# Kernel optimization log

Hardware: AMD Instinct MI355X
Metric: run time of the kernel (lower is better)

The kernel has to match this reference:

```python
import jax, jax.numpy as jnp
import numpy as np

B, NF, S, L, H, MID, KS, NC, DENSE = 16, 8, 16, 256, 128, 32, 8, 10, 512
COEFF = 0.1
BN_EPS = 1e-5


def _normalize(x):
    return x / jnp.maximum(jnp.linalg.norm(x, axis=-1, keepdims=True), 1e-12)


def _sparsemax(z):
    # sparsemax over last axis (Martins & Astudillo 2016)
    zs = jnp.flip(jnp.sort(z, axis=-1), axis=-1)
    k = jnp.arange(1, z.shape[-1] + 1, dtype=z.dtype)
    cum = jnp.cumsum(zs, axis=-1)
    support = (1.0 + k * zs) > cum
    ksup = jnp.sum(support, axis=-1, keepdims=True)
    tau = (jnp.take_along_axis(cum, ksup - 1, axis=-1) - 1.0) / ksup.astype(z.dtype)
    return jnp.maximum(z - tau, 0.0)


def _bn_ncl(x, g, b, m, v):  # eval-mode BatchNorm1d on [N, C, L]
    return g[None, :, None] * (x - m[None, :, None]) * jax.lax.rsqrt(v[None, :, None] + BN_EPS) + b[None, :, None]


def _bn_nc(x, g, b, m, v):  # eval-mode BatchNorm1d on [N, C]
    return g * (x - m) * jax.lax.rsqrt(v + BN_EPS) + b


def _conv(x, w, pad):
    return jax.lax.conv_general_dilated(x, w, (1,), [(pad, pad)], dimension_numbers=('NCH', 'OIH', 'NCH'))


def _maxpool2(x):  # MaxPool1d(kernel=2, stride=2, padding=1): -inf padded
    return jax.lax.reduce_window(x, -jnp.inf, jax.lax.max, (1, 1, 2), (1, 1, 2), ((0, 0), (0, 0), (1, 1)))


def _cnn(x, cw1, bn1, cw2, bn2, cw3, bn3):
    x = _maxpool2(jax.nn.relu(_bn_ncl(_conv(x, cw1, KS // 2), *bn1)))
    x = _maxpool2(jax.nn.relu(_bn_ncl(_conv(x, cw2, 4), *bn2)))
    x = _maxpool2(jax.nn.relu(_bn_ncl(_conv(x, cw3, 4), *bn3)))
    return jnp.mean(x, axis=-1)  # AdaptiveAvgPool1d(1) -> [N, H]


def _alpha_beta(x, cw1, bn1, cw2, bn2, cw3, bn3, Wq, bq, Wk, bk, Wv, bv):
    b = x.shape[0]
    xf = jnp.transpose(x, (1, 0, 2, 3)).reshape(NF, b * S, 1, L)
    rep = jax.vmap(_cnn)(xf, cw1, bn1, cw2, bn2, cw3, bn3)  # [F, B*S, H]
    rep = rep.reshape(NF, b, S, H)
    Q = jax.nn.elu(rep @ Wq + bq)
    K = jax.nn.leaky_relu(rep @ Wk + bk)
    V = jax.nn.leaky_relu(rep @ Wv + bv)
    # mean_t(Q @ K^T) == Q @ mean_t(K); then scale by sqrt(d_k)
    scores = jnp.einsum('fbsh,fbh->fbs', Q, jnp.mean(K, axis=2)) / jnp.sqrt(jnp.float32(H))
    intra_aw = _sparsemax(scores)                             # [F, B, S]
    Z = _normalize(jnp.einsum('fbs,fbsh->fbh', intra_aw, V))  # [F, B, H]
    Kn = _normalize(rep)
    inter_scores = jnp.einsum('ibh,fbsh->ifbs', Z, Kn)        # cosine scores (Z already unit-norm)
    inter_aw = _sparsemax(inter_scores)                       # [I, F, B, S]
    U = jnp.einsum('ifbs,fbsh->ibh', inter_aw, rep) / NF      # mean over feature axis f
    Hc = _normalize(jnp.concatenate([Z, U], axis=-1))         # [F, B, 2H]
    feat = jnp.transpose(Hc, (1, 0, 2)).reshape(b, NF * 2 * H)
    return feat, intra_aw, inter_aw


def _forward(src_x, src_y, tgt_x, cw1, bn1_g, bn1_b, bn1_m, bn1_v, cw2, bn2_g, bn2_b, bn2_m, bn2_v, cw3, bn3_g, bn3_b, bn3_m, bn3_v, Wq, bq, Wk, bk, Wv, bv, bnc1_g, bnc1_b, bnc1_m, bnc1_v, W1, b1, bnc2_g, bnc2_b, bnc2_m, bnc2_v, W2, b2):
    bn1 = (bn1_g, bn1_b, bn1_m, bn1_v)
    bn2 = (bn2_g, bn2_b, bn2_m, bn2_v)
    bn3 = (bn3_g, bn3_b, bn3_m, bn3_v)
    sf, sa, sb = _alpha_beta(src_x, cw1, bn1, cw2, bn2, cw3, bn3, Wq, bq, Wk, bk, Wv, bv)
    _, ta, tb = _alpha_beta(tgt_x, cw1, bn1, cw2, bn2, cw3, bn3, Wq, bq, Wk, bk, Wv, bv)
    h = _bn_nc(sf, bnc1_g, bnc1_b, bnc1_m, bnc1_v) @ W1 + b1
    h = jax.nn.leaky_relu(_bn_nc(h, bnc2_g, bnc2_b, bnc2_m, bnc2_v))
    y_pred = jax.nn.softmax(h @ W2 + b2, axis=-1)
    # MMD domain losses (detached in original via torch.tensor(list))
    da = jnp.mean(sa - ta, axis=-2)                           # [F, S]
    loss_a = COEFF * jnp.mean(jnp.linalg.norm(da, axis=-1))
    db = jnp.mean(sb - tb, axis=-2)                           # [I, F, S]
    loss_b = COEFF * jnp.mean(jnp.sqrt(jnp.sum(db * db, axis=(1, 2))))
    dom = jax.lax.stop_gradient(loss_a + loss_b)
    # CrossEntropyLoss applied to already-softmaxed preds, as in source
    logp = jax.nn.log_softmax(y_pred, axis=-1)
    ce = -jnp.mean(logp[jnp.arange(y_pred.shape[0]), src_y])
    return y_pred, ce + dom


def setup_inputs() -> dict:
    ks = jax.random.split(jax.random.key(0), 40)
    rn = lambda i, sh, s=1.0: s * jax.random.normal(ks[i], sh, dtype=jnp.float32)
    ru = lambda i, sh, lo, hi: jax.random.uniform(ks[i], sh, jnp.float32, lo, hi)
    return {
        'src_x': rn(0, (B, NF, S, L)),
        'src_y': jax.random.randint(ks[1], (B,), 0, NC),
        'tgt_x': rn(2, (B, NF, S, L)),
        'cw1': rn(3, (NF, MID, 1, KS), 0.1),
        'bn1_g': ru(4, (NF, MID), 0.75, 1.25), 'bn1_b': rn(5, (NF, MID), 0.1),
        'bn1_m': rn(6, (NF, MID), 0.1), 'bn1_v': ru(7, (NF, MID), 0.5, 1.5),
        'cw2': rn(8, (NF, 2 * MID, MID, 8), 0.05),
        'bn2_g': ru(9, (NF, 2 * MID), 0.75, 1.25), 'bn2_b': rn(10, (NF, 2 * MID), 0.1),
        'bn2_m': rn(11, (NF, 2 * MID), 0.1), 'bn2_v': ru(12, (NF, 2 * MID), 0.5, 1.5),
        'cw3': rn(13, (NF, H, 2 * MID, 8), 0.05),
        'bn3_g': ru(14, (NF, H), 0.75, 1.25), 'bn3_b': rn(15, (NF, H), 0.1),
        'bn3_m': rn(16, (NF, H), 0.1), 'bn3_v': ru(17, (NF, H), 0.5, 1.5),
        'Wq': rn(18, (H, H), 0.05), 'bq': rn(19, (H,), 0.02),
        'Wk': rn(20, (H, H), 0.05), 'bk': rn(21, (H,), 0.02),
        'Wv': rn(22, (H, H), 0.05), 'bv': rn(23, (H,), 0.02),
        'bnc1_g': ru(24, (NF * 2 * H,), 0.75, 1.25), 'bnc1_b': rn(25, (NF * 2 * H,), 0.1),
        'bnc1_m': rn(26, (NF * 2 * H,), 0.1), 'bnc1_v': ru(27, (NF * 2 * H,), 0.5, 1.5),
        'W1': rn(28, (NF * 2 * H, DENSE), 0.03), 'b1': rn(29, (DENSE,), 0.02),
        'bnc2_g': ru(30, (DENSE,), 0.75, 1.25), 'bnc2_b': rn(31, (DENSE,), 0.1),
        'bnc2_m': rn(32, (DENSE,), 0.1), 'bnc2_v': ru(33, (DENSE,), 0.5, 1.5),
        'W2': rn(34, (DENSE, NC), 0.05), 'b2': rn(35, (NC,), 0.02),
    }


def reference(src_x, src_y, tgt_x, cw1, bn1_g, bn1_b, bn1_m, bn1_v, cw2, bn2_g, bn2_b, bn2_m, bn2_v, cw3, bn3_g, bn3_b, bn3_m, bn3_v, Wq, bq, Wk, bk, Wv, bv, bnc1_g, bnc1_b, bnc1_m, bnc1_v, W1, b1, bnc2_g, bnc2_b, bnc2_m, bnc2_v, W2, b2):
    return _forward(src_x, src_y, tgt_x, cw1, bn1_g, bn1_b, bn1_m, bn1_v, cw2, bn2_g, bn2_b, bn2_m, bn2_v, cw3, bn3_g, bn3_b, bn3_m, bn3_v, Wq, bq, Wk, bk, Wv, bv, bnc1_g, bnc1_b, bnc1_m, bnc1_v, W1, b1, bnc2_g, bnc2_b, bnc2_m, bnc2_v, W2, b2)
```

## Files before the change

kernel.cpp:

```cpp
#include <hip/hip_runtime.h>

typedef unsigned short u16;
typedef unsigned int u32;
typedef __attribute__((ext_vector_type(8))) short bfrag;
typedef __attribute__((ext_vector_type(4))) float ffrag;

__device__ __forceinline__ float lrelu(float x) { return x >= 0.f ? x : 0.01f * x; }
__device__ __forceinline__ float eluf(float x)  { return x > 0.f ? x : expm1f(x); }
__device__ __forceinline__ u16 f2bf(float f) {
    u32 x = __float_as_uint(f);
    return (u16)((x + 0x7fffu + ((x >> 16) & 1u)) >> 16);
}
__device__ __forceinline__ u16 f2bt(float f) {
    return (u16)(__float_as_uint(f) >> 16);
}
__device__ __forceinline__ float bf2f(u16 u) {
    return __uint_as_float(((u32)u) << 16);
}

__device__ void sparsemax16(const float* z, float* out) {
    float zs[16];
    for (int i = 0; i < 16; ++i) zs[i] = z[i];
    for (int i = 1; i < 16; ++i) {
        float key = zs[i]; int j = i - 1;
        while (j >= 0 && zs[j] < key) { zs[j + 1] = zs[j]; --j; }
        zs[j + 1] = key;
    }
    float cum[16];
    cum[0] = zs[0];
    for (int i = 1; i < 16; ++i) cum[i] = cum[i - 1] + zs[i];
    int ksup = 0;
    for (int k = 1; k <= 16; ++k)
        if (1.0f + (float)k * zs[k - 1] > cum[k - 1]) ksup++;
    if (ksup < 1) ksup = 1;
    float tau = (cum[ksup - 1] - 1.0f) / (float)ksup;
    for (int i = 0; i < 16; ++i) out[i] = fmaxf(z[i] - tau, 0.0f);
}

__global__ __launch_bounds__(256) void k_wprep(
    const float* __restrict__ w2, const float* __restrict__ w3,
    const float* __restrict__ Wq, const float* __restrict__ Wk,
    const float* __restrict__ Wv,
    u16* __restrict__ wpk2, u16* __restrict__ wpk3, u16* __restrict__ wqkv)
{
    int i = blockIdx.x * 256 + threadIdx.x;
    if (i < 131072) {
        int j = i & 7, L = (i >> 3) & 63, kc = (i >> 9) & 7, nt = (i >> 12) & 3, f = i >> 14;
        int co = nt * 16 + (L & 15);
        int ci = ((L >> 4) << 3) + j;
        wpk2[i] = f2bf(w2[(((size_t)f * 64 + co) * 32 + ci) * 8 + kc]);
    } else if (i < 131072 + 524288) {
        int i2 = i - 131072;
        int j = i2 & 7, L = (i2 >> 3) & 63, kc = (i2 >> 9) & 15, nt = (i2 >> 13) & 7, f = i2 >> 16;
        int co = nt * 16 + (L & 15);
        int ci = ((kc & 1) << 5) + ((L >> 4) << 3) + j;
        wpk3[i2] = f2bf(w3[(((size_t)f * 128 + co) * 64 + ci) * 8 + (kc >> 1)]);
    } else if (i < 131072 + 524288 + 49152) {
        int j2 = i - 655360;
        int proj = j2 >> 14, idx = j2 & 16383;
        int jj = idx & 7, L = (idx >> 3) & 63, kc = (idx >> 9) & 3, nt = idx >> 11;
        int n = nt * 16 + (L & 15);
        int k = kc * 32 + ((L >> 4) << 3) + jj;
        const float* W = proj == 0 ? Wq : (proj == 1 ? Wk : Wv);
        wqkv[j2] = f2bf(W[k * 128 + n]);
    }
}

#define S1T_STRIDE 40
#define S2T_STRIDE 72
#define RB2_STRIDE 68
#define RB3_STRIDE 140
#define RB_OFF 6336
#define SMEM_U16 (RB_OFF + 67 * RB3_STRIDE)

__global__ __launch_bounds__(256) void k_cnn(
    const float* __restrict__ xs, const float* __restrict__ xt,
    const float* __restrict__ w1, const float* __restrict__ g1, const float* __restrict__ b1,
    const float* __restrict__ m1, const float* __restrict__ v1,
    const float* __restrict__ g2, const float* __restrict__ b2,
    const float* __restrict__ m2, const float* __restrict__ v2,
    const float* __restrict__ g3, const float* __restrict__ b3,
    const float* __restrict__ m3, const float* __restrict__ v3,
    const u16* __restrict__ wpk2, const u16* __restrict__ wpk3,
    float* __restrict__ rep)
{
    __shared__ __align__(16) u16 smem[SMEM_U16];
    float* xin = (float*)(smem + RB_OFF);

    int tid = threadIdx.x, blk = blockIdx.x;
    int pass = blk >> 11, f = (blk >> 8) & 7, n = blk & 255;
    int bb = n >> 4, ss = n & 15;
    int lane = tid & 63, w = tid >> 6;
    const float* x = pass ? xt : xs;
    float* rep_p = rep + (size_t)pass * 262144;

    {
        u32* z = (u32*)smem;
        for (int i = tid; i < 3168; i += 256) z[i] = 0;
        for (int i = tid; i < 264; i += 256) xin[i] = 0.f;
    }
    __syncthreads();
    {
        const float* xr = x + (((size_t)bb * 8 + f) * 16 + ss) * 256;
        for (int i = tid; i < 256; i += 256) xin[i + 4] = xr[i];
    }
    __syncthreads();

    if (tid < 208) {
        int cc = tid & 7, jc = tid >> 3;
        int co0 = cc * 4, j0 = jc * 5;
        float wr[4][8];
        for (int c = 0; c < 4; ++c) {
            const float4* q = reinterpret_cast<const float4*>(w1 + ((size_t)f * 32 + co0 + c) * 8);
            float4 a = q[0], bq = q[1];
            wr[c][0] = a.x; wr[c][1] = a.y; wr[c][2] = a.z; wr[c][3] = a.w;
            wr[c][4] = bq.x; wr[c][5] = bq.y; wr[c][6] = bq.z; wr[c][7] = bq.w;
        }
        int px[10];
        for (int i = 0; i < 10; ++i) {
            int p = 2 * j0 - 1 + i;
            px[i] = p < 0 ? 0 : (p > 256 ? 256 : p);
        }
        float acc[4][10];
        for (int c = 0; c < 4; ++c) for (int i = 0; i < 10; ++i) acc[c][i] = 0.f;
        for (int k = 0; k < 8; ++k) {
            float xv[10];
            for (int i = 0; i < 10; ++i) xv[i] = xin[px[i] + k];
            for (int c = 0; c < 4; ++c)
                for (int i = 0; i < 10; ++i) acc[c][i] += wr[c][k] * xv[i];
        }
        for (int c = 0; c < 4; ++c) {
            int co = co0 + c;
            float sc = g1[f * 32 + co] * rsqrtf(v1[f * 32 + co] + 1e-5f);
            float sh = b1[f * 32 + co] - m1[f * 32 + co] * sc;
            for (int jj = 0; jj < 5; ++jj) {
                int j = j0 + jj;
                if (j < 129) {
                    float a0 = fmaxf(acc[c][2 * jj] * sc + sh, 0.f);
                    float a1 = fmaxf(acc[c][2 * jj + 1] * sc + sh, 0.f);
                    smem[(j + 4) * S1T_STRIDE + co] = f2bt(fmaxf(a0, a1));
                }
            }
        }
    }
    __syncthreads();

    {
        int nt = w;
        bfrag B2[8];
        const bfrag* gB = reinterpret_cast<const bfrag*>(wpk2);
        for (int kc = 0; kc < 8; ++kc)
            B2[kc] = gB[(((size_t)f * 4 + nt) * 8 + kc) * 64 + lane];
        int co = nt * 16 + (lane & 15);
        float sc = g2[f * 64 + co] * rsqrtf(v2[f * 64 + co] + 1e-5f);
        float sh = b2[f * 64 + co] - m2[f * 64 + co] * sc;
        int arow = lane & 15, ci0 = (lane >> 4) << 3;
        for (int mt = 0; mt < 9; ++mt) {
            ffrag C = {0.f, 0.f, 0.f, 0.f};
            int rb = mt * 16 + arow;
            for (int kc = 0; kc < 8; ++kc) {
                bfrag A = *reinterpret_cast<const bfrag*>(&smem[(rb + kc) * S1T_STRIDE + ci0]);
                C = __builtin_amdgcn_mfma_f32_16x16x32_bf16(A, B2[kc], C, 0, 0, 0);
            }
            int p0 = mt * 16 + ((lane >> 4) << 2);
            for (int r = 0; r < 4; ++r) {
                int p = p0 + r;
                if (p < 130)
                    smem[RB_OFF + p * RB2_STRIDE + co] = f2bt(fmaxf(C[r] * sc + sh, 0.f));
            }
        }
    }
    __syncthreads();

    {
        u32* z = (u32*)smem;
        for (int i = tid; i < 3168; i += 256) z[i] = 0;
    }
    __syncthreads();

    for (int e = tid; e < 66 * 64; e += 256) {
        int j = e >> 6, ci = e & 63;
        float vmax;
        if (j == 0) {
            vmax = bf2f(smem[RB_OFF + 0 * RB2_STRIDE + ci]);
        } else if (j == 65) {
            vmax = bf2f(smem[RB_OFF + 129 * RB2_STRIDE + ci]);
        } else {
            float a0 = bf2f(smem[RB_OFF + (2 * j - 1) * RB2_STRIDE + ci]);
            float a1 = bf2f(smem[RB_OFF + (2 * j) * RB2_STRIDE + ci]);
            vmax = fmaxf(a0, a1);
        }
        smem[(j + 4) * S2T_STRIDE + ci] = f2bt(vmax);
    }
    __syncthreads();

    for (int t = 0; t < 2; ++t) {
        int nt = w * 2 + t;
        bfrag B3[16];
        const bfrag* gB = reinterpret_cast<const bfrag*>(wpk3);
        for (int kc = 0; kc < 16; ++kc)
            B3[kc] = gB[(((size_t)f * 8 + nt) * 16 + kc) * 64 + lane];
        int co = nt * 16 + (lane & 15);
        float sc = g3[f * 128 + co] * rsqrtf(v3[f * 128 + co] + 1e-5f);
        float sh = b3[f * 128 + co] - m3[f * 128 + co] * sc;
        int arow = lane & 15, q8 = (lane >> 4) << 3;
        for (int mt = 0; mt < 5; ++mt) {
            ffrag C = {0.f, 0.f, 0.f, 0.f};
            int rb = mt * 16 + arow;
            for (int kc = 0; kc < 16; ++kc) {
                int row = rb + (kc >> 1);
                int ci0 = ((kc & 1) << 5) + q8;
                bfrag A = *reinterpret_cast<const bfrag*>(&smem[row * S2T_STRIDE + ci0]);
                C = __builtin_amdgcn_mfma_f32_16x16x32_bf16(A, B3[kc], C, 0, 0, 0);
            }
            int p0 = mt * 16 + ((lane >> 4) << 2);
            for (int r = 0; r < 4; ++r) {
                int p = p0 + r;
                if (p < 67)
                    smem[RB_OFF + p * RB3_STRIDE + co] = f2bt(fmaxf(C[r] * sc + sh, 0.f));
            }
        }
    }
    __syncthreads();

    if (tid < 128) {
        int co = tid;
        float sum = bf2f(smem[RB_OFF + 0 * RB3_STRIDE + co]);
        for (int j = 1; j < 34; ++j) {
            float a0 = bf2f(smem[RB_OFF + (2 * j - 1) * RB3_STRIDE + co]);
            float a1 = bf2f(smem[RB_OFF + (2 * j) * RB3_STRIDE + co]);
            sum += fmaxf(a0, a1);
        }
        rep_p[(((size_t)f * 256) + n) * 128 + co] = sum * (1.0f / 34.0f);
    }
}

__global__ __launch_bounds__(256) void k_attn1(
    const float* __restrict__ rep, const u16* __restrict__ wqkv,
    const float* __restrict__ bq, const float* __restrict__ bk,
    const float* __restrict__ bv,
    float* __restrict__ Zn, float* __restrict__ rninv, float* __restrict__ iaw)
{
    __shared__ __align__(16) u16 repbf[16 * 136];
    __shared__ float KmL[128], ZL[128], awL[16], scoresL[16], r2L[16];
    __shared__ float spart[4][4][4];
    __shared__ float redL[4];
    int tid = threadIdx.x;
    int pass = blockIdx.x >> 7, f = (blockIdx.x >> 4) & 7, b = blockIdx.x & 15;
    const float* rp = rep + (size_t)pass * 262144 + ((size_t)f * 256 + b * 16) * 128;
    float* Zn_p = Zn + (size_t)pass * 16384;
    float* rninv_p = rninv + (size_t)pass * 2048;
    float* iaw_p = iaw + (size_t)pass * 2048;

    {
        int s = tid >> 4, i = tid & 15, h0 = i * 8;
        const float4* q4 = reinterpret_cast<const float4*>(rp + s * 128 + h0);
        float4 a = q4[0], c = q4[1];
        float p2 = a.x*a.x + a.y*a.y + a.z*a.z + a.w*a.w
                 + c.x*c.x + c.y*c.y + c.z*c.z + c.w*c.w;
        bfrag pk;
        pk[0] = (short)f2bt(a.x); pk[1] = (short)f2bt(a.y);
        pk[2] = (short)f2bt(a.z); pk[3] = (short)f2bt(a.w);
        pk[4] = (short)f2bt(c.x); pk[5] = (short)f2bt(c.y);
        pk[6] = (short)f2bt(c.z); pk[7] = (short)f2bt(c.w);
        *reinterpret_cast<bfrag*>(&repbf[s * 136 + h0]) = pk;
        p2 += __shfl_xor(p2, 1); p2 += __shfl_xor(p2, 2);
        p2 += __shfl_xor(p2, 4); p2 += __shfl_xor(p2, 8);
        if (i == 0) r2L[s] = p2;
    }
    __syncthreads();

    int lane = tid & 63, w = tid >> 6, arow = lane & 15, q = lane >> 4;
    bfrag A[4];
    for (int kc = 0; kc < 4; ++kc)
        A[kc] = *reinterpret_cast<const bfrag*>(&repbf[arow * 136 + kc * 32 + q * 8]);

    float qv[2][4], vvv[2][4];
    int colv[2];
    const bfrag* BB = reinterpret_cast<const bfrag*>(wqkv);
    for (int t = 0; t < 2; ++t) {
        int nt = w * 2 + t;
        ffrag cq = {0.f,0.f,0.f,0.f}, ck = {0.f,0.f,0.f,0.f}, cv = {0.f,0.f,0.f,0.f};
        for (int kc = 0; kc < 4; ++kc) {
            int fi = (nt * 4 + kc) * 64 + lane;
            bfrag Bq = BB[fi];
            bfrag Bk = BB[2048 + fi];
            bfrag Bv = BB[4096 + fi];
            cq = __builtin_amdgcn_mfma_f32_16x16x32_bf16(A[kc], Bq, cq, 0, 0, 0);
            ck = __builtin_amdgcn_mfma_f32_16x16x32_bf16(A[kc], Bk, ck, 0, 0, 0);
            cv = __builtin_amdgcn_mfma_f32_16x16x32_bf16(A[kc], Bv, cv, 0, 0, 0);
        }
        int col = nt * 16 + arow;
        colv[t] = col;
        float bqc = bq[col], bkc = bk[col], bvc = bv[col];
        float kpt = 0.f;
        for (int r = 0; r < 4; ++r) {
            qv[t][r] = eluf(cq[r] + bqc);
            vvv[t][r] = lrelu(cv[r] + bvc);
            kpt += lrelu(ck[r] + bkc);
        }
        kpt += __shfl_xor(kpt, 16);
        kpt += __shfl_xor(kpt, 32);
        if (q == 0) KmL[col] = kpt * (1.f / 16.f);
    }
    __syncthreads();

    {
        float km0 = KmL[colv[0]], km1 = KmL[colv[1]];
        float ps[4];
        for (int r = 0; r < 4; ++r) {
            float v = qv[0][r] * km0 + qv[1][r] * km1;
            v += __shfl_xor(v, 1); v += __shfl_xor(v, 2);
            v += __shfl_xor(v, 4); v += __shfl_xor(v, 8);
            ps[r] = v;
        }
        if (arow == 0)
            for (int r = 0; r < 4; ++r) spart[w][q][r] = ps[r];
    }
    __syncthreads();
    if (tid < 16) {
        int qq = tid >> 2, rr = tid & 3;
        float sc = spart[0][qq][rr] + spart[1][qq][rr] + spart[2][qq][rr] + spart[3][qq][rr];
        scoresL[tid] = sc * 0.08838834764831845f;
        rninv_p[f * 256 + b * 16 + tid] = 1.f / fmaxf(sqrtf(r2L[tid]), 1e-12f);
    }
    __syncthreads();
    if (tid == 0) sparsemax16(scoresL, awL);
    __syncthreads();
    if (tid < 16) iaw_p[f * 256 + b * 16 + tid] = awL[tid];

    for (int t = 0; t < 2; ++t) {
        float zp = 0.f;
        for (int r = 0; r < 4; ++r) zp += awL[q * 4 + r] * vvv[t][r];
        zp += __shfl_xor(zp, 16);
        zp += __shfl_xor(zp, 32);
        if (q == 0) ZL[colv[t]] = zp;
    }
    __syncthreads();
    if (tid < 128) {
        float z = ZL[tid];
        float v = z * z;
        v += __shfl_xor(v, 1); v += __shfl_xor(v, 2); v += __shfl_xor(v, 4);
        v += __shfl_xor(v, 8); v += __shfl_xor(v, 16); v += __shfl_xor(v, 32);
        if (lane == 0) redL[w] = v;
    }
    __syncthreads();
    if (tid == 0) redL[2] = 1.f / fmaxf(sqrtf(redL[0] + redL[1]), 1e-12f);
    __syncthreads();
    if (tid < 128)
        Zn_p[((size_t)f * 16 + b) * 128 + tid] = ZL[tid] * redL[2];
}

__global__ __launch_bounds__(256) void k_attn2(
    const float* __restrict__ rep, const float* __restrict__ Zn,
    const float* __restrict__ rninv, float* __restrict__ ibw,
    const float* __restrict__ g, const float* __restrict__ bb,
    const float* __restrict__ mm, const float* __restrict__ vv,
    float* __restrict__ featbn)
{
    __shared__ float repL[16384];
    __shared__ float ZiL[128], scores[128], UL[128];
    __shared__ float awLf[8][16];
    __shared__ float redL[2];
    int tid = threadIdx.x, blk = blockIdx.x;
    int pass = blk >> 7, b = (blk >> 3) & 15, i = blk & 7;
    const float* rep_p = rep + (size_t)pass * 262144;

    for (int f = 0; f < 8; ++f) {
        const float4* src = reinterpret_cast<const float4*>(
            rep_p + ((size_t)f * 256 + b * 16) * 128);
        float4* dst = reinterpret_cast<float4*>(repL + f * 2048);
        for (int t = tid; t < 512; t += 256) dst[t] = src[t];
    }
    if (tid < 128) ZiL[tid] = Zn[(size_t)pass * 16384 + ((size_t)i * 16 + b) * 128 + tid];
    __syncthreads();

    if (tid < 128) {
        int f = tid >> 4, s = tid & 15;
        const float* rr = repL + tid * 128;
        float a = 0.f;
        for (int h = 0; h < 128; ++h) a += ZiL[h] * rr[h];
        scores[tid] = a * rninv[(size_t)pass * 2048 + f * 256 + b * 16 + s];
    }
    __syncthreads();
    if (tid < 8) {
        float aw[16];
        sparsemax16(&scores[tid * 16], aw);
        for (int s = 0; s < 16; ++s) awLf[tid][s] = aw[s];
    }
    __syncthreads();
    if (tid < 128) {
        int f = tid >> 4, s = tid & 15;
        ibw[(size_t)pass * 16384 + (((size_t)i * 8 + f) * 16 + b) * 16 + s] = awLf[f][s];
    }
    if (pass == 0) {
        if (tid < 128) {
            int h = tid;
            float u = 0.f;
            for (int f = 0; f < 8; ++f) {
                const float* rr = repL + f * 2048 + h;
                const float* aa = awLf[f];
                for (int s = 0; s < 16; ++s) u += aa[s] * rr[s * 128];
            }
            UL[h] = u * 0.125f;
        }
        __syncthreads();
        if (tid < 128) {
            int lane = tid & 63, w = tid >> 6;
            float v = ZiL[tid] * ZiL[tid] + UL[tid] * UL[tid];
            v += __shfl_xor(v, 1); v += __shfl_xor(v, 2); v += __shfl_xor(v, 4);
            v += __shfl_xor(v, 8); v += __shfl_xor(v, 16); v += __shfl_xor(v, 32);
            if (lane == 0) redL[w] = v;
        }
        __syncthreads();
        if (tid < 256) {
            float inv = 1.f / fmaxf(sqrtf(redL[0] + redL[1]), 1e-12f);
            int d = tid;
            int e = i * 256 + d;
            float val = (d < 128 ? ZiL[d] : UL[d - 128]) * inv;
            float scv = g[e] * rsqrtf(vv[e] + 1e-5f);
            featbn[b * 2048 + e] = (val - mm[e]) * scv + bb[e];
        }
    }
}

__global__ __launch_bounds__(256) void k_head1(
    const float* __restrict__ featbn,
    const float* __restrict__ W1, const float* __restrict__ b1,
    const float* __restrict__ g2, const float* __restrict__ bb2,
    const float* __restrict__ mm2, const float* __restrict__ vv2,
    float* __restrict__ h2ws)
{
    __shared__ float featL[2048];
    __shared__ float part[32][32];
    int tid = threadIdx.x, blk = blockIdx.x;
    int b = blk >> 4, cc = blk & 15;
    {
        const float4* src = reinterpret_cast<const float4*>(featbn + b * 2048);
        float4* dst = reinterpret_cast<float4*>(featL);
        for (int i = tid; i < 512; i += 256) dst[i] = src[i];
    }
    __syncthreads();
    int ks = tid >> 3, cg = tid & 7;
    int col0 = cc * 32 + cg * 4;
    float4 acc = {0.f, 0.f, 0.f, 0.f};
    const float* fl = featL + ks * 64;
    for (int c = 0; c < 64; ++c) {
        int k = ks * 64 + c;
        float4 wv = *reinterpret_cast<const float4*>(W1 + (size_t)k * 512 + col0);
        float fv = fl[c];
        acc.x += fv * wv.x; acc.y += fv * wv.y;
        acc.z += fv * wv.z; acc.w += fv * wv.w;
    }
    part[ks][cg * 4 + 0] = acc.x;
    part[ks][cg * 4 + 1] = acc.y;
    part[ks][cg * 4 + 2] = acc.z;
    part[ks][cg * 4 + 3] = acc.w;
    __syncthreads();
    if (tid < 32) {
        int colw = cc * 32 + tid;
        float s = b1[colw];
        for (int k2 = 0; k2 < 32; ++k2) s += part[k2][tid];
        float scv = g2[colw] * rsqrtf(vv2[colw] + 1e-5f);
        float val = (s - mm2[colw]) * scv + bb2[colw];
        h2ws[b * 512 + colw] = lrelu(val);
    }
}

__global__ __launch_bounds__(256) void k_tail(
    const float* __restrict__ h2ws,
    const float* __restrict__ W2, const float* __restrict__ b2,
    const float* __restrict__ sa, const float* __restrict__ ta,
    const float* __restrict__ sb, const float* __restrict__ tb,
    const int* __restrict__ sy, float* __restrict__ dout)
{
    __shared__ float h2L[8192];
    __shared__ float lgL[160], ypL[160];
    __shared__ float sA[8], sB[8];
    int tid = threadIdx.x;
    for (int i = tid; i < 8192; i += 256) h2L[i] = h2ws[i];
    if (tid < 8) { sA[tid] = 0.f; sB[tid] = 0.f; }
    __syncthreads();
    if (tid < 160) {
        int b = tid / 10, j = tid - b * 10;
        float a = b2[j];
        const float* h = h2L + b * 512;
        for (int c = 0; c < 512; ++c) a += h[c] * W2[c * 10 + j];
        lgL[tid] = a;
    }
    __syncthreads();
    if (tid < 16) {
        int b = tid;
        float mx = lgL[b * 10];
        for (int j = 1; j < 10; ++j) mx = fmaxf(mx, lgL[b * 10 + j]);
        float sum = 0.f, ex[10];
        for (int j = 0; j < 10; ++j) { ex[j] = expf(lgL[b * 10 + j] - mx); sum += ex[j]; }
        for (int j = 0; j < 10; ++j) {
            float p = ex[j] / sum;
            ypL[b * 10 + j] = p;
            dout[b * 10 + j] = p;
        }
    }
    __syncthreads();
    if (tid < 128) {
        int f = tid >> 4, s = tid & 15;
        float d = 0.f;
        for (int b = 0; b < 16; ++b) d += sa[f * 256 + b * 16 + s] - ta[f * 256 + b * 16 + s];
        d *= (1.f / 16.f);
        atomicAdd(&sA[f], d * d);
    }
    for (int e = tid; e < 1024; e += 256) {
        int i = e >> 7, f = (e >> 4) & 7, s = e & 15;
        float d = 0.f;
        int base = ((i * 8 + f) * 16) * 16 + s;
        for (int b = 0; b < 16; ++b) d += sb[base + b * 16] - tb[base + b * 16];
        d *= (1.f / 16.f);
        atomicAdd(&sB[i], d * d);
    }
    __syncthreads();
    if (tid == 0) {
        float la = 0.f, lb = 0.f;
        for (int f = 0; f < 8; ++f) la += sqrtf(sA[f]);
        for (int i = 0; i < 8; ++i) lb += sqrtf(sB[i]);
        la *= 0.1f / 8.f;
        lb *= 0.1f / 8.f;
        float ce = 0.f;
        for (int b = 0; b < 16; ++b) {
            const float* y = ypL + b * 10;
            float mx = y[0];
            for (int j = 1; j < 10; ++j) mx = fmaxf(mx, y[j]);
            float sum = 0.f;
            for (int j = 0; j < 10; ++j) sum += expf(y[j] - mx);
            float lse = mx + logf(sum);
            ce += lse - y[sy[b]];
        }
        ce *= (1.f / 16.f);
        dout[160] = ce + la + lb;
    }
}

extern "C" void kernel_launch(void* const* d_in, const int* in_sizes, int n_in,
                              void* d_out, int out_size, void* d_ws, size_t ws_size,
                              hipStream_t stream) {
    (void)in_sizes; (void)n_in; (void)out_size; (void)ws_size;
    const float* src_x = (const float*)d_in[0];
    const int*   src_y = (const int*)d_in[1];
    const float* tgt_x = (const float*)d_in[2];
    const float *cw1 = (const float*)d_in[3], *bn1g = (const float*)d_in[4],
                *bn1b = (const float*)d_in[5], *bn1m = (const float*)d_in[6],
                *bn1v = (const float*)d_in[7];
    const float *cw2 = (const float*)d_in[8], *bn2g = (const float*)d_in[9],
                *bn2b = (const float*)d_in[10], *bn2m = (const float*)d_in[11],
                *bn2v = (const float*)d_in[12];
    const float *cw3 = (const float*)d_in[13], *bn3g = (const float*)d_in[14],
                *bn3b = (const float*)d_in[15], *bn3m = (const float*)d_in[16],
                *bn3v = (const float*)d_in[17];
    const float *Wq = (const float*)d_in[18], *bq = (const float*)d_in[19],
                *Wk = (const float*)d_in[20], *bk = (const float*)d_in[21],
                *Wv = (const float*)d_in[22], *bv = (const float*)d_in[23];
    const float *bc1g = (const float*)d_in[24], *bc1b = (const float*)d_in[25],
                *bc1m = (const float*)d_in[26], *bc1v = (const float*)d_in[27];
    const float *W1 = (const float*)d_in[28], *b1 = (const float*)d_in[29];
    const float *bc2g = (const float*)d_in[30], *bc2b = (const float*)d_in[31],
                *bc2m = (const float*)d_in[32], *bc2v = (const float*)d_in[33];
    const float *W2 = (const float*)d_in[34], *b2 = (const float*)d_in[35];

    float* ws = (float*)d_ws;
    size_t o = 0;
    float* rep    = ws + o; o += (size_t)2 * 262144;
    float* Zn     = ws + o; o += (size_t)2 * 16384;
    float* rninv  = ws + o; o += (size_t)2 * 2048;
    float* ia     = ws + o; o += (size_t)2 * 2048;
    float* ib     = ws + o; o += (size_t)2 * 16384;
    float* featbn = ws + o; o += (size_t)16 * 2048;
    float* h2ws   = ws + o; o += (size_t)16 * 512;
    u16* wpk2 = (u16*)(ws + o); o += 65536;
    u16* wpk3 = (u16*)(ws + o); o += 262144;
    u16* wqkv = (u16*)(ws + o); o += 24576;

    k_wprep<<<2752, 256, 0, stream>>>(cw2, cw3, Wq, Wk, Wv, wpk2, wpk3, wqkv);
    k_cnn<<<4096, 256, 0, stream>>>(src_x, tgt_x,
        cw1, bn1g, bn1b, bn1m, bn1v,
        bn2g, bn2b, bn2m, bn2v,
        bn3g, bn3b, bn3m, bn3v,
        wpk2, wpk3, rep);
    k_attn1<<<256, 256, 0, stream>>>(rep, wqkv, bq, bk, bv, Zn, rninv, ia);
    k_attn2<<<256, 256, 0, stream>>>(rep, Zn, rninv, ib, bc1g, bc1b, bc1m, bc1v, featbn);
    k_head1<<<256, 256, 0, stream>>>(featbn, W1, b1, bc2g, bc2b, bc2m, bc2v, h2ws);
    k_tail<<<1, 256, 0, stream>>>(h2ws, W2, b2, ia, ia + 2048, ib, ib + 16384,
                                  src_y, (float*)d_out);
}
```

Before: 314.9 us.

## Fuse maxpool and mean into MFMA epilogues using cross-lane shuffles

```diff
diff --git a/kernel.cpp b/kernel.cpp
--- a/kernel.cpp
+++ b/kernel.cpp
@@ -66,12 +66,12 @@
     }
 }
 
-#define S1T_STRIDE 40
-#define S2T_STRIDE 72
-#define RB2_STRIDE 68
-#define RB3_STRIDE 140
-#define RB_OFF 6336
-#define SMEM_U16 (RB_OFF + 67 * RB3_STRIDE)
+#define S1_BASE 0
+#define S1_STRIDE 40
+#define S2_BASE 6040
+#define S2_STRIDE 72
+#define XIN_U16 12304
+#define SMEM_U16 12832
 
 __global__ __launch_bounds__(256) void k_cnn(
     const float* __restrict__ xs, const float* __restrict__ xt,
@@ -85,22 +85,23 @@
     float* __restrict__ rep)
 {
     __shared__ __align__(16) u16 smem[SMEM_U16];
-    float* xin = (float*)(smem + RB_OFF);
+    float* xin = (float*)(smem + XIN_U16);
 
     int tid = threadIdx.x, blk = blockIdx.x;
     int pass = blk >> 11, f = (blk >> 8) & 7, n = blk & 255;
     int bb = n >> 4, ss = n & 15;
     int lane = tid & 63, w = tid >> 6;
+    int arow = lane & 15, q = lane >> 4;
     const float* x = pass ? xt : xs;
     float* rep_p = rep + (size_t)pass * 262144;
 
     {
         u32* z = (u32*)smem;
-        for (int i = tid; i < 3168; i += 256) z[i] = 0;
-        for (int i = tid; i < 264; i += 256) xin[i] = 0.f;
-    }
-    __syncthreads();
-    {
+        for (int i = tid; i < 80; i += 256) z[i] = 0;
+        for (int i = tid; i < 360; i += 256) z[2660 + i] = 0;
+        for (int i = tid; i < 144; i += 256) z[3020 + i] = 0;
+        for (int i = tid; i < 612; i += 256) z[3020 + 2520 + i] = 0;
+        if (tid < 4) { xin[tid] = 0.f; xin[260 + tid] = 0.f; }
         const float* xr = x + (((size_t)bb * 8 + f) * 16 + ss) * 256;
         for (int i = tid; i < 256; i += 256) xin[i + 4] = xr[i];
     }
@@ -111,8 +112,8 @@
         int co0 = cc * 4, j0 = jc * 5;
         float wr[4][8];
         for (int c = 0; c < 4; ++c) {
-            const float4* q = reinterpret_cast<const float4*>(w1 + ((size_t)f * 32 + co0 + c) * 8);
-            float4 a = q[0], bq = q[1];
+            const float4* qq = reinterpret_cast<const float4*>(w1 + ((size_t)f * 32 + co0 + c) * 8);
+            float4 a = qq[0], bq = qq[1];
             wr[c][0] = a.x; wr[c][1] = a.y; wr[c][2] = a.z; wr[c][3] = a.w;
             wr[c][4] = bq.x; wr[c][5] = bq.y; wr[c][6] = bq.z; wr[c][7] = bq.w;
         }
@@ -138,7 +139,7 @@
                 if (j < 129) {
                     float a0 = fmaxf(acc[c][2 * jj] * sc + sh, 0.f);
                     float a1 = fmaxf(acc[c][2 * jj + 1] * sc + sh, 0.f);
-                    smem[(j + 4) * S1T_STRIDE + co] = f2bt(fmaxf(a0, a1));
+                    smem[(j + 4) * S1_STRIDE + co] = f2bt(fmaxf(a0, a1));
                 }
             }
         }
@@ -151,46 +152,31 @@
         const bfrag* gB = reinterpret_cast<const bfrag*>(wpk2);
         for (int kc = 0; kc < 8; ++kc)
             B2[kc] = gB[(((size_t)f * 4 + nt) * 8 + kc) * 64 + lane];
-        int co = nt * 16 + (lane & 15);
+        int co = nt * 16 + arow;
         float sc = g2[f * 64 + co] * rsqrtf(v2[f * 64 + co] + 1e-5f);
         float sh = b2[f * 64 + co] - m2[f * 64 + co] * sc;
-        int arow = lane & 15, ci0 = (lane >> 4) << 3;
+        int ci0 = q << 3;
+        float carry = -INFINITY;
         for (int mt = 0; mt < 9; ++mt) {
             ffrag C = {0.f, 0.f, 0.f, 0.f};
             int rb = mt * 16 + arow;
             for (int kc = 0; kc < 8; ++kc) {
-                bfrag A = *reinterpret_cast<const bfrag*>(&smem[(rb + kc) * S1T_STRIDE + ci0]);
+                bfrag A = *reinterpret_cast<const bfrag*>(&smem[(rb + kc) * S1_STRIDE + ci0]);
                 C = __builtin_amdgcn_mfma_f32_16x16x32_bf16(A, B2[kc], C, 0, 0, 0);
             }
-            int p0 = mt * 16 + ((lane >> 4) << 2);
-            for (int r = 0; r < 4; ++r) {
-                int p = p0 + r;
-                if (p < 130)
-                    smem[RB_OFF + p * RB2_STRIDE + co] = f2bt(fmaxf(C[r] * sc + sh, 0.f));
-            }
-        }
-    }
-    __syncthreads();
-
-    {
-        u32* z = (u32*)smem;
-        for (int i = tid; i < 3168; i += 256) z[i] = 0;
-    }
-    __syncthreads();
-
-    for (int e = tid; e < 66 * 64; e += 256) {
-        int j = e >> 6, ci = e & 63;
-        float vmax;
-        if (j == 0) {
-            vmax = bf2f(smem[RB_OFF + 0 * RB2_STRIDE + ci]);
-        } else if (j == 65) {
-            vmax = bf2f(smem[RB_OFF + 129 * RB2_STRIDE + ci]);
-        } else {
-            float a0 = bf2f(smem[RB_OFF + (2 * j - 1) * RB2_STRIDE + ci]);
-            float a1 = bf2f(smem[RB_OFF + (2 * j) * RB2_STRIDE + ci]);
-            vmax = fmaxf(a0, a1);
-        }
-        smem[(j + 4) * S2T_STRIDE + ci] = f2bt(vmax);
+            int p0 = mt * 16 + (q << 2);
+            float v0 = (p0 < 130) ? fmaxf(C[0] * sc + sh, 0.f) : -INFINITY;
+            float v1 = (p0 + 1 < 130) ? fmaxf(C[1] * sc + sh, 0.f) : -INFINITY;
+            float v2c = (p0 + 2 < 130) ? fmaxf(C[2] * sc + sh, 0.f) : -INFINITY;
+            float v3 = (p0 + 3 < 130) ? fmaxf(C[3] * sc + sh, 0.f) : -INFINITY;
+            float up = __shfl_up(v3, 16);
+            float pc = __shfl(carry, 48 + arow);
+            float prev = (q == 0) ? pc : up;
+            carry = v3;
+            int ja = p0 >> 1, jb = ja + 1;
+            if (ja < 66) smem[S2_BASE + (ja + 4) * S2_STRIDE + co] = f2bt(fmaxf(prev, v0));
+            if (jb < 66) smem[S2_BASE + (jb + 4) * S2_STRIDE + co] = f2bt(fmaxf(v1, v2c));
+        }
     }
     __syncthreads();
 
@@ -200,38 +186,38 @@
         const bfrag* gB = reinterpret_cast<const bfrag*>(wpk3);
         for (int kc = 0; kc < 16; ++kc)
             B3[kc] = gB[(((size_t)f * 8 + nt) * 16 + kc) * 64 + lane];
-        int co = nt * 16 + (lane & 15);
+        int co = nt * 16 + arow;
         float sc = g3[f * 128 + co] * rsqrtf(v3[f * 128 + co] + 1e-5f);
         float sh = b3[f * 128 + co] - m3[f * 128 + co] * sc;
-        int arow = lane & 15, q8 = (lane >> 4) << 3;
+        int q8 = q << 3;
+        float carry = -INFINITY;
+        float msum = 0.f;
         for (int mt = 0; mt < 5; ++mt) {
             ffrag C = {0.f, 0.f, 0.f, 0.f};
             int rb = mt * 16 + arow;
             for (int kc = 0; kc < 16; ++kc) {
                 int row = rb + (kc >> 1);
                 int ci0 = ((kc & 1) << 5) + q8;
-                bfrag A = *reinterpret_cast<const bfrag*>(&smem[row * S2T_STRIDE + ci0]);
+                bfrag A = *reinterpret_cast<const bfrag*>(&smem[S2_BASE + row * S2_STRIDE + ci0]);
                 C = __builtin_amdgcn_mfma_f32_16x16x32_bf16(A, B3[kc], C, 0, 0, 0);
             }
-            int p0 = mt * 16 + ((lane >> 4) << 2);
-            for (int r = 0; r < 4; ++r) {
-                int p = p0 + r;
-                if (p < 67)
-                    smem[RB_OFF + p * RB3_STRIDE + co] = f2bt(fmaxf(C[r] * sc + sh, 0.f));
-            }
-        }
-    }
-    __syncthreads();
-
-    if (tid < 128) {
-        int co = tid;
-        float sum = bf2f(smem[RB_OFF + 0 * RB3_STRIDE + co]);
-        for (int j = 1; j < 34; ++j) {
-            float a0 = bf2f(smem[RB_OFF + (2 * j - 1) * RB3_STRIDE + co]);
-            float a1 = bf2f(smem[RB_OFF + (2 * j) * RB3_STRIDE + co]);
-            sum += fmaxf(a0, a1);
-        }
-        rep_p[(((size_t)f * 256) + n) * 128 + co] = sum * (1.0f / 34.0f);
+            int p0 = mt * 16 + (q << 2);
+            float v0 = (p0 < 67) ? fmaxf(C[0] * sc + sh, 0.f) : -INFINITY;
+            float v1 = (p0 + 1 < 67) ? fmaxf(C[1] * sc + sh, 0.f) : -INFINITY;
+            float v2c = (p0 + 2 < 67) ? fmaxf(C[2] * sc + sh, 0.f) : -INFINITY;
+            float v3c = (p0 + 3 < 67) ? fmaxf(C[3] * sc + sh, 0.f) : -INFINITY;
+            float up = __shfl_up(v3c, 16);
+            float pc = __shfl(carry, 48 + arow);
+            float prev = (q == 0) ? pc : up;
+            carry = v3c;
+            int ja = p0 >> 1, jb = ja + 1;
+            if (ja < 34) msum += bf2f(f2bt(fmaxf(prev, v0)));
+            if (jb < 34) msum += bf2f(f2bt(fmaxf(v1, v2c)));
+        }
+        msum += __shfl_xor(msum, 16);
+        msum += __shfl_xor(msum, 32);
+        if (q == 0)
+            rep_p[(((size_t)f * 256) + n) * 128 + co] = msum * (1.0f / 34.0f);
     }
 }
 
```

Result: slower. 427.9 us (+35.9%).
